# Kernel optimization log

Measured on AMD Instinct MI355X. Metric: run time of the kernel, lower is better.

## Reference

```python
import jax, jax.numpy as jnp
import numpy as np

B, C_IN, C_OUT, N, K = 8, 64, 128, 2048, 16
EPS = 1e-5  # torch BatchNorm2d default


def setup_inputs() -> dict:
    key = jax.random.key(0)
    ks = jax.random.split(key, 2)
    x = jax.random.normal(ks[0], (B, C_IN, N, 1), dtype=jnp.float32)
    # Conv2d(2*C_IN, C_OUT, 1) kaiming_normal weight, zero bias; 1x1 kernel -> [C_OUT, 2*C_IN]
    W = jax.random.normal(ks[1], (C_OUT, 2 * C_IN), dtype=jnp.float32) * np.float32(np.sqrt(2.0 / (2 * C_IN)))
    b = jnp.zeros((C_OUT,), jnp.float32)
    gamma = jnp.ones((C_OUT,), jnp.float32)   # BN weight filled with 1
    beta = jnp.zeros((C_OUT,), jnp.float32)   # BN bias zeroed
    return {"x": x, "W": W, "b": b, "gamma": gamma, "beta": beta, "k": K}


def reference(x, W, b, gamma, beta, k):
    # x: [B, C, N, 1]
    xs = x[..., 0]                              # [B, C, N]
    feats = jnp.transpose(xs, (0, 2, 1))        # [B, N, C]
    # knn: pairwise_distance = -||xi||^2 + 2 xi.xj - ||xj||^2 (negative sq dist)
    sq = jnp.sum(xs * xs, axis=1)               # [B, N]
    gram = jnp.einsum('bcn,bcm->bnm', xs, xs)   # [B, N, N]
    pd = 2.0 * gram - sq[:, :, None] - sq[:, None, :]
    idx = jax.lax.top_k(pd, k)[1]               # [B, N, k] neighbor indices
    # gather: x_j = neighbor features, x_i = center features broadcast over k
    x_j = jnp.take_along_axis(feats[:, None, :, :], idx[:, :, :, None], axis=2)  # [B, N, k, C]
    x_i = feats[:, :, None, :]                  # [B, N, 1, C]
    e = jnp.concatenate([jnp.broadcast_to(x_i, x_j.shape), x_j - x_i], axis=-1)  # [B, N, k, 2C]
    # 1x1 conv (matmul over channels) + ReLU
    h = jax.nn.relu(jnp.einsum('bnkc,oc->bnko', e, W) + b)  # [B, N, k, O]
    # BatchNorm2d in training mode: batch stats over (B, N, k), biased variance
    mean = jnp.mean(h, axis=(0, 1, 2))
    var = jnp.mean(jnp.square(h - mean), axis=(0, 1, 2))
    h = (h - mean) * jax.lax.rsqrt(var + EPS) * gamma + beta
    # max over neighbors, back to [B, O, N, 1]
    out = jnp.max(h, axis=2)                    # [B, N, O]
    return jnp.transpose(out, (0, 2, 1))[..., None]
```

## Files before the change

kernel.cpp:

```cpp
#include <hip/hip_runtime.h>
#include <math.h>

#define BB 8
#define CIN 64
#define CO 128
#define NPT 2048
#define KK 16
#define EPSV 1e-5f
#define LOSCALE 2048.0f

typedef unsigned int u32;
typedef unsigned long long u64;
typedef _Float16 f16x8 __attribute__((ext_vector_type(8)));
typedef float f32x4 __attribute__((ext_vector_type(4)));

__global__ __launch_bounds__(256) void k_prep_pv(
    const float* __restrict__ x, const float* __restrict__ W,
    const float* __restrict__ bias, float* __restrict__ sq,
    _Float16* __restrict__ xh, _Float16* __restrict__ xl,
    float* __restrict__ p, float* __restrict__ v) {
  __shared__ float tile[64][65];
  __shared__ float tileT[64][68];
  __shared__ float psum[4][64];
  int bid = blockIdx.x;
  int b = bid >> 5;
  int n0 = (bid & 31) << 6;
  int tid = threadIdx.x;
  int q = tid >> 6, lo = tid & 63;
#pragma unroll
  for (int i = 0; i < 16; ++i) {
    int c = i * 4 + q;
    tile[c][lo] = x[((size_t)(b * CIN + c)) * NPT + n0 + lo];
  }
  __syncthreads();
  float ps = 0.f;
#pragma unroll
  for (int i = 0; i < 16; ++i) {
    float t = tile[q * 16 + i][lo];
    ps += t * t;
  }
  psum[q][lo] = ps;
#pragma unroll
  for (int i = 0; i < 16; ++i) {
    int ni = i * 4 + q;
    float val = tile[lo][ni];
    tileT[ni][lo] = val;
    size_t o = ((size_t)(b * NPT + n0 + ni)) * CIN + lo;
    _Float16 h = (_Float16)val;
    xh[o] = h;
    xl[o] = (_Float16)((val - (float)h) * LOSCALE);
  }
  __syncthreads();
  if (q == 0) {
    sq[(size_t)b * NPT + n0 + lo] = psum[0][lo] + psum[1][lo] + psum[2][lo] + psum[3][lo];
  }
  int o = tid & 127, hh = tid >> 7;
  const float4* W1 = (const float4*)&W[o * 2 * CIN];
  const float4* W2 = (const float4*)&W[o * 2 * CIN + CIN];
  float bo = bias[o];
#pragma unroll 2
  for (int t = 0; t < 32; ++t) {
    int node = t * 2 + hh;
    float a1 = 0.f, a2 = 0.f;
#pragma unroll
    for (int c4 = 0; c4 < 16; ++c4) {
      float4 xv = *(const float4*)&tileT[node][c4 * 4];
      float4 w1 = W1[c4];
      float4 w2 = W2[c4];
      a1 += xv.x * w1.x + xv.y * w1.y + xv.z * w1.z + xv.w * w1.w;
      a2 += xv.x * w2.x + xv.y * w2.y + xv.z * w2.z + xv.w * w2.w;
    }
    size_t gn = ((size_t)(b * NPT + n0 + node)) * CO + o;
    p[gn] = a1 - a2 + bo;
    v[gn] = a2;
  }
}

__global__ __launch_bounds__(1024) void k_dist_topk(
    const _Float16* __restrict__ xh, const _Float16* __restrict__ xl,
    const float* __restrict__ sq, float* p_mx,
    const float* __restrict__ v, float* __restrict__ psums,
    float* __restrict__ psqs) {
  __shared__ uint4 tiles[16][2][256];
  __shared__ float submax[16][64];
  __shared__ float2 cand[16][96];
  __shared__ int cnt[16];
  __shared__ float tauf[16];

  int bid = (blockIdx.x & 7) * 128 + (blockIdx.x >> 3);
  int b = bid >> 7;
  int rt = (bid & 127) << 4;
  int tid = threadIdx.x;
  int w = tid >> 6, lane = tid & 63;
  int lr = lane & 15, lg = lane >> 4;
  const _Float16* xhb = xh + (size_t)b * NPT * CIN;
  const _Float16* xlb = xl + (size_t)b * NPT * CIN;
  const float* sqb = sq + (size_t)b * NPT;

  if (tid < 16) cnt[tid] = 0;

  const size_t arow = (size_t)(rt + lr) * CIN + lg * 8;
  f16x8 ah0 = *(const f16x8*)(xhb + arow);
  f16x8 ah1 = *(const f16x8*)(xhb + arow + 32);
  f16x8 al0 = *(const f16x8*)(xlb + arow);
  f16x8 al1 = *(const f16x8*)(xlb + arow + 32);
  float4 sqr = *(const float4*)(sqb + rt + lg * 4);
  float sqrv[4] = {sqr.x, sqr.y, sqr.z, sqr.w};
  float csqs[8];
#pragma unroll
  for (int t = 0; t < 8; ++t) csqs[t] = sqb[(w * 8 + t) * 16 + lr];

  const char* xhB = (const char*)xhb;
  const char* xlB = (const char*)xlb;
  const int su = (lane ^ ((lane >> 3) & 7)) * 16;

#define ISSUE_TILE(T)                                                          \
  {                                                                            \
    const int tb_ = (w * 8 + (T)) * 2048;                                      \
    uint4* buf_ = &tiles[w][(T) & 1][0];                                       \
    __builtin_amdgcn_global_load_lds((const uint4*)(xhB + tb_ + su),           \
                                     buf_, 16, 0, 0);                          \
    __builtin_amdgcn_global_load_lds((const uint4*)(xhB + tb_ + 1024 + su),    \
                                     buf_ + 64, 16, 0, 0);                     \
    __builtin_amdgcn_global_load_lds((const uint4*)(xlB + tb_ + su),           \
                                     buf_ + 128, 16, 0, 0);                    \
    __builtin_amdgcn_global_load_lds((const uint4*)(xlB + tb_ + 1024 + su),    \
                                     buf_ + 192, 16, 0, 0);                    \
  }

  ISSUE_TILE(0)
  ISSUE_TILE(1)

  const int uh0 = lr * 8 + (lg ^ (lr & 7));
  const int uh1 = lr * 8 + ((lg + 4) ^ (lr & 7));
  float vals[32];

#pragma unroll
  for (int t = 0; t < 8; ++t) {
    if (t < 7) { asm volatile("s_waitcnt vmcnt(4)" ::: "memory"); }
    else       { asm volatile("s_waitcnt vmcnt(0)" ::: "memory"); }
    __builtin_amdgcn_sched_barrier(0);
    const uint4* bufr = &tiles[w][t & 1][0];
    f16x8 bh0 = *(const f16x8*)(bufr + uh0);
    f16x8 bh1 = *(const f16x8*)(bufr + uh1);
    f16x8 bl0 = *(const f16x8*)(bufr + 128 + uh0);
    f16x8 bl1 = *(const f16x8*)(bufr + 128 + uh1);
    asm volatile("s_waitcnt lgkmcnt(0)" ::: "memory");
    __builtin_amdgcn_sched_barrier(0);
    if (t == 0) ISSUE_TILE(2)
    if (t == 1) ISSUE_TILE(3)
    if (t == 2) ISSUE_TILE(4)
    if (t == 3) ISSUE_TILE(5)
    if (t == 4) ISSUE_TILE(6)
    if (t == 5) ISSUE_TILE(7)
    f32x4 acc0 = {0.f, 0.f, 0.f, 0.f};
    f32x4 acc1 = {0.f, 0.f, 0.f, 0.f};
    acc1 = __builtin_amdgcn_mfma_f32_16x16x32_f16(ah0, bl0, acc1, 0, 0, 0);
    acc1 = __builtin_amdgcn_mfma_f32_16x16x32_f16(al0, bh0, acc1, 0, 0, 0);
    acc1 = __builtin_amdgcn_mfma_f32_16x16x32_f16(ah1, bl1, acc1, 0, 0, 0);
    acc1 = __builtin_amdgcn_mfma_f32_16x16x32_f16(al1, bh1, acc1, 0, 0, 0);
    acc0 = __builtin_amdgcn_mfma_f32_16x16x32_f16(ah0, bh0, acc0, 0, 0, 0);
    acc0 = __builtin_amdgcn_mfma_f32_16x16x32_f16(ah1, bh1, acc0, 0, 0, 0);
    const float k2 = 2.0f / LOSCALE;
#pragma unroll
    for (int q = 0; q < 4; ++q) {
      vals[t * 4 + q] = fmaf(acc1[q], k2, 2.f * acc0[q]) - (sqrv[q] + csqs[t]);
    }
  }
#undef ISSUE_TILE

  float rmax[4];
#pragma unroll
  for (int q = 0; q < 4; ++q) {
    float m = vals[q];
#pragma unroll
    for (int t = 1; t < 8; ++t) m = fmaxf(m, vals[t * 4 + q]);
    m = fmaxf(m, __shfl_xor(m, 1, 64));
    m = fmaxf(m, __shfl_xor(m, 2, 64));
    rmax[q] = m;
  }
  if ((lr & 3) == 0) {
    int pool = w * 4 + (lr >> 2);
#pragma unroll
    for (int q = 0; q < 4; ++q) submax[lg * 4 + q][pool] = rmax[q];
  }
  __syncthreads();

  {
    u32 ou = __float_as_uint(submax[w][lane]);
    ou = (ou & 0x80000000u) ? ~ou : (ou | 0x80000000u);
    u32 lo = 0u;
#pragma unroll
    for (int s2 = 31; s2 >= 16; --s2) {
      u32 cd = lo | (1u << s2);
      u64 bal = __ballot(ou >= cd);
      if (__popcll(bal) >= KK) lo = cd;
    }
    u32 tb = (lo & 0x80000000u) ? (lo ^ 0x80000000u) : ~lo;
    if (lane == 0) tauf[w] = __uint_as_float(tb);
  }
  __syncthreads();

  {
    float tq[4];
#pragma unroll
    for (int q = 0; q < 4; ++q) tq[q] = tauf[lg * 4 + q];
#pragma unroll
    for (int t = 0; t < 8; ++t) {
#pragma unroll
      for (int q = 0; q < 4; ++q) {
        float vv = vals[t * 4 + q];
        if (vv >= tq[q]) {
          int r = lg * 4 + q;
          int pos = atomicAdd(&cnt[r], 1);
          if (pos < 96) cand[r][pos] = make_float2(vv, __int_as_float((w * 8 + t) * 16 + lr));
        }
      }
    }
  }
  __syncthreads();

  int total = cnt[w];
  if (total > 96) total = 96;
  const float NINF = -__builtin_inff();
  float cv = NINF;
  int ci = 0x7FFFFFFF;
  int n1 = total < 64 ? total : 64;
  if (lane < n1) {
    float2 pr = cand[w][lane];
    cv = pr.x; ci = __float_as_int(pr.y);
  }

#define PSORT(KMAX)                                                        \
  _Pragma("unroll") for (int k = 2; k <= (KMAX); k <<= 1) {                \
    _Pragma("unroll") for (int j = k >> 1; j > 0; j >>= 1) {               \
      float pv = __shfl_xor(cv, j, 64);                                    \
      int pi = __shfl_xor(ci, j, 64);                                      \
      bool up = (lane & k) != 0;                                           \
      bool lw = (lane & j) == 0;                                           \
      bool gt = (cv > pv) || (cv == pv && ci < pi);                        \
      bool keep = (lw != up) ? gt : !gt;                                   \
      cv = keep ? cv : pv;                                                 \
      ci = keep ? ci : pi;                                                 \
    }                                                                      \
  }

  if (total > 32) {
    PSORT(64)
    if (total > 64) {
      if (lane >= 16) {
        int src2 = 48 + lane;
        if (src2 < total) {
          float2 pr = cand[w][src2];
          cv = pr.x; ci = __float_as_int(pr.y);
        } else { cv = NINF; ci = 0x7FFFFFFF; }
      }
      PSORT(64)
    }
  } else {
    PSORT(32)
  }
#undef PSORT

  {
    int jj[16];
#pragma unroll
    for (int k = 0; k < KK; ++k) jj[k] = __shfl(ci, k, 64) & (NPT - 1);
    size_t gn = (size_t)(b * NPT + rt + w);
    const float* vb = v + (size_t)b * NPT * CO;
    float2 p2 = *(const float2*)(p_mx + gn * CO + lane * 2);
    float2 s2 = {0.f, 0.f}, q2 = {0.f, 0.f}, m2 = {-1e30f, -1e30f};
#pragma unroll
    for (int k = 0; k < KK; ++k) {
      float2 v2 = *(const float2*)(vb + (size_t)jj[k] * CO + lane * 2);
      float h0 = fmaxf(p2.x + v2.x, 0.f);
      float h1 = fmaxf(p2.y + v2.y, 0.f);
      s2.x += h0; s2.y += h1;
      q2.x += h0 * h0; q2.y += h1 * h1;
      m2.x = fmaxf(m2.x, h0); m2.y = fmaxf(m2.y, h1);
    }
    *(float2*)(p_mx + gn * CO + lane * 2) = m2;
    float* sp = (float*)tiles;
    *(float2*)(sp + w * 128 + lane * 2) = s2;
    *(float2*)(sp + 2048 + w * 128 + lane * 2) = q2;
  }
  __syncthreads();
  if (tid < CO) {
    float* sp = (float*)tiles;
    float ts = 0.f, tq = 0.f;
#pragma unroll
    for (int i = 0; i < 16; ++i) { ts += sp[i * 128 + tid]; tq += sp[2048 + i * 128 + tid]; }
    int obid = b * 128 + (rt >> 4);
    psums[(size_t)obid * CO + tid] = ts;
    psqs[(size_t)obid * CO + tid] = tq;
  }
}

__global__ __launch_bounds__(64) void k_final(
    const float* __restrict__ psums, const float* __restrict__ psqs,
    const float* __restrict__ gamma, const float* __restrict__ beta,
    float* __restrict__ scale, float* __restrict__ shift) {
  int o = blockIdx.x;
  int t = threadIdx.x;
  float s = 0.f, q = 0.f;
  for (int i = t; i < BB * (NPT / 16); i += 64) {
    s += psums[(size_t)i * CO + o];
    q += psqs[(size_t)i * CO + o];
  }
#pragma unroll
  for (int d = 32; d >= 1; d >>= 1) {
    s += __shfl_down(s, d, 64);
    q += __shfl_down(q, d, 64);
  }
  if (t == 0) {
    const float M = (float)(BB * NPT * KK);
    float mean = s / M;
    float var = q / M - mean * mean;
    float sc = gamma[o] * rsqrtf(var + EPSV);
    scale[o] = sc;
    shift[o] = beta[o] - mean * sc;
  }
}

__global__ __launch_bounds__(256) void k_out_fast(
    const float* __restrict__ mxb, const float* __restrict__ scale,
    const float* __restrict__ shift, float* __restrict__ out) {
  __shared__ float ob[32][132];
  int bid = blockIdx.x;
  int b = bid >> 6;
  int n0 = (bid & 63) << 5;
  int tid = threadIdx.x;
  int o4 = tid & 31, ns = tid >> 5;
  float4 sc = *(const float4*)(scale + o4 * 4);
  float4 sh = *(const float4*)(shift + o4 * 4);
#pragma unroll
  for (int g = 0; g < 4; ++g) {
    int node = g * 8 + ns;
    size_t po = (size_t)(b * NPT + n0 + node) * CO + o4 * 4;
    float4 mx = *(const float4*)(mxb + po);
    float4 r;
    r.x = mx.x * sc.x + sh.x;
    r.y = mx.y * sc.y + sh.y;
    r.z = mx.z * sc.z + sh.z;
    r.w = mx.w * sc.w + sh.w;
    *(float4*)&ob[node][o4 * 4] = r;
  }
  __syncthreads();
  int ni = tid & 31, oh = tid >> 5;
#pragma unroll
  for (int pass = 0; pass < 16; ++pass) {
    int o = pass * 8 + oh;
    out[((size_t)(b * CO + o)) * NPT + n0 + ni] = ob[ni][o];
  }
}

extern "C" void kernel_launch(void* const* d_in, const int* in_sizes, int n_in,
                              void* d_out, int out_size, void* d_ws, size_t ws_size,
                              hipStream_t stream) {
  const float* x = (const float*)d_in[0];
  const float* W = (const float*)d_in[1];
  const float* bias = (const float*)d_in[2];
  const float* gamma = (const float*)d_in[3];
  const float* beta = (const float*)d_in[4];
  float* out = (float*)d_out;

  char* ws = (char*)d_ws;
  size_t off = 0;
  auto alloc = [&](size_t bytes) {
    void* ptr = ws + off;
    off += (bytes + 255) & ~(size_t)255;
    return ptr;
  };
  _Float16* xh = (_Float16*)alloc(sizeof(_Float16) * BB * NPT * CIN);
  _Float16* xl = (_Float16*)alloc(sizeof(_Float16) * BB * NPT * CIN);
  float* sq = (float*)alloc(sizeof(float) * BB * NPT);
  float* p = (float*)alloc(sizeof(float) * BB * NPT * CO);
  float* v = (float*)alloc(sizeof(float) * BB * NPT * CO);
  float* psums = (float*)alloc(sizeof(float) * BB * (NPT / 16) * CO);
  float* psqs = (float*)alloc(sizeof(float) * BB * (NPT / 16) * CO);
  float* scale = (float*)alloc(sizeof(float) * CO);
  float* shift = (float*)alloc(sizeof(float) * CO);
  (void)ws_size; (void)in_sizes; (void)n_in; (void)out_size;

  hipLaunchKernelGGL(k_prep_pv, dim3(BB * (NPT / 64)), dim3(256), 0, stream,
                     x, W, bias, sq, xh, xl, p, v);
  hipLaunchKernelGGL(k_dist_topk, dim3(BB * (NPT / 16)), dim3(1024), 0, stream,
                     xh, xl, sq, p, v, psums, psqs);
  hipLaunchKernelGGL(k_final, dim3(CO), dim3(64), 0, stream, psums, psqs, gamma, beta, scale, shift);
  hipLaunchKernelGGL(k_out_fast, dim3(BB * (NPT / 32)), dim3(256), 0, stream, p, scale, shift, out);
}
```

Baseline: 107.4 us.

## Compute per-point conv projections with split-fp16 MFMA instead of scalar FMA

The per-point linear projections p = (W1-W2)x + b and v = W2 x move from a scalar fp32 dot-product loop to MFMA 16x16x32 f16 instructions. Both operands are split into hi/lo fp16 parts to approximate fp32 accuracy, and the lo*lo term is dropped. A new small kernel pre-splits the weights (W1-W2 and W2) into hi/lo fp16 once per call. This cuts the scalar FLOP cost in k_prep_pv and removes the transposed fp32 LDS tile. The cost is an extra kernel launch and slightly reduced precision from the dropped cross term.

```diff
diff --git a/kernel.cpp b/kernel.cpp
--- a/kernel.cpp
+++ b/kernel.cpp
@@ -14,14 +14,33 @@
 typedef _Float16 f16x8 __attribute__((ext_vector_type(8)));
 typedef float f32x4 __attribute__((ext_vector_type(4)));
 
+__global__ __launch_bounds__(256) void k_wsplit(
+    const float* __restrict__ W, _Float16* __restrict__ wdh,
+    _Float16* __restrict__ wdl, _Float16* __restrict__ w2h,
+    _Float16* __restrict__ w2l) {
+  int i = blockIdx.x * 256 + threadIdx.x;
+  int o = i >> 6, c = i & 63;
+  float w1 = W[o * 2 * CIN + c];
+  float w2 = W[o * 2 * CIN + CIN + c];
+  float wd = w1 - w2;
+  _Float16 h2 = (_Float16)w2;
+  w2h[i] = h2;
+  w2l[i] = (_Float16)((w2 - (float)h2) * LOSCALE);
+  _Float16 hd = (_Float16)wd;
+  wdh[i] = hd;
+  wdl[i] = (_Float16)((wd - (float)hd) * LOSCALE);
+}
+
 __global__ __launch_bounds__(256) void k_prep_pv(
-    const float* __restrict__ x, const float* __restrict__ W,
-    const float* __restrict__ bias, float* __restrict__ sq,
-    _Float16* __restrict__ xh, _Float16* __restrict__ xl,
-    float* __restrict__ p, float* __restrict__ v) {
+    const float* __restrict__ x, const float* __restrict__ bias,
+    const _Float16* __restrict__ wdh, const _Float16* __restrict__ wdl,
+    const _Float16* __restrict__ w2h, const _Float16* __restrict__ w2l,
+    float* __restrict__ sq, _Float16* __restrict__ xh,
+    _Float16* __restrict__ xl, float* __restrict__ p, float* __restrict__ v) {
   __shared__ float tile[64][65];
-  __shared__ float tileT[64][68];
   __shared__ float psum[4][64];
+  __shared__ _Float16 xhp[64][72];
+  __shared__ _Float16 xlp[64][72];
   int bid = blockIdx.x;
   int b = bid >> 5;
   int n0 = (bid & 31) << 6;
@@ -44,35 +63,58 @@
   for (int i = 0; i < 16; ++i) {
     int ni = i * 4 + q;
     float val = tile[lo][ni];
-    tileT[ni][lo] = val;
     size_t o = ((size_t)(b * NPT + n0 + ni)) * CIN + lo;
     _Float16 h = (_Float16)val;
+    _Float16 l = (_Float16)((val - (float)h) * LOSCALE);
     xh[o] = h;
-    xl[o] = (_Float16)((val - (float)h) * LOSCALE);
-  }
-  __syncthreads();
+    xl[o] = l;
+    xhp[ni][lo] = h;
+    xlp[ni][lo] = l;
+  }
   if (q == 0) {
     sq[(size_t)b * NPT + n0 + lo] = psum[0][lo] + psum[1][lo] + psum[2][lo] + psum[3][lo];
   }
-  int o = tid & 127, hh = tid >> 7;
-  const float4* W1 = (const float4*)&W[o * 2 * CIN];
-  const float4* W2 = (const float4*)&W[o * 2 * CIN + CIN];
-  float bo = bias[o];
-#pragma unroll 2
-  for (int t = 0; t < 32; ++t) {
-    int node = t * 2 + hh;
-    float a1 = 0.f, a2 = 0.f;
-#pragma unroll
-    for (int c4 = 0; c4 < 16; ++c4) {
-      float4 xv = *(const float4*)&tileT[node][c4 * 4];
-      float4 w1 = W1[c4];
-      float4 w2 = W2[c4];
-      a1 += xv.x * w1.x + xv.y * w1.y + xv.z * w1.z + xv.w * w1.w;
-      a2 += xv.x * w2.x + xv.y * w2.y + xv.z * w2.z + xv.w * w2.w;
-    }
-    size_t gn = ((size_t)(b * NPT + n0 + node)) * CO + o;
-    p[gn] = a1 - a2 + bo;
-    v[gn] = a2;
+  __syncthreads();
+
+  int w = tid >> 6, lane = tid & 63;
+  int lr = lane & 15, lg = lane >> 4;
+  f16x8 ah0 = *(const f16x8*)&xhp[w * 16 + lr][lg * 8];
+  f16x8 ah1 = *(const f16x8*)&xhp[w * 16 + lr][lg * 8 + 32];
+  f16x8 al0 = *(const f16x8*)&xlp[w * 16 + lr][lg * 8];
+  f16x8 al1 = *(const f16x8*)&xlp[w * 16 + lr][lg * 8 + 32];
+  const float kinv = 1.0f / LOSCALE;
+#pragma unroll 1
+  for (int ot = 0; ot < 8; ++ot) {
+    int orow = ot * 16 + lr;
+    const f16x8 bdh0 = *(const f16x8*)(wdh + orow * 64 + lg * 8);
+    const f16x8 bdh1 = *(const f16x8*)(wdh + orow * 64 + lg * 8 + 32);
+    const f16x8 bdl0 = *(const f16x8*)(wdl + orow * 64 + lg * 8);
+    const f16x8 bdl1 = *(const f16x8*)(wdl + orow * 64 + lg * 8 + 32);
+    const f16x8 b2h0 = *(const f16x8*)(w2h + orow * 64 + lg * 8);
+    const f16x8 b2h1 = *(const f16x8*)(w2h + orow * 64 + lg * 8 + 32);
+    const f16x8 b2l0 = *(const f16x8*)(w2l + orow * 64 + lg * 8);
+    const f16x8 b2l1 = *(const f16x8*)(w2l + orow * 64 + lg * 8 + 32);
+    float bo = bias[orow];
+    f32x4 pa0 = {0.f, 0.f, 0.f, 0.f}, pa1 = {0.f, 0.f, 0.f, 0.f};
+    f32x4 va0 = {0.f, 0.f, 0.f, 0.f}, va1 = {0.f, 0.f, 0.f, 0.f};
+    pa1 = __builtin_amdgcn_mfma_f32_16x16x32_f16(ah0, bdl0, pa1, 0, 0, 0);
+    pa1 = __builtin_amdgcn_mfma_f32_16x16x32_f16(al0, bdh0, pa1, 0, 0, 0);
+    pa1 = __builtin_amdgcn_mfma_f32_16x16x32_f16(ah1, bdl1, pa1, 0, 0, 0);
+    pa1 = __builtin_amdgcn_mfma_f32_16x16x32_f16(al1, bdh1, pa1, 0, 0, 0);
+    pa0 = __builtin_amdgcn_mfma_f32_16x16x32_f16(ah0, bdh0, pa0, 0, 0, 0);
+    pa0 = __builtin_amdgcn_mfma_f32_16x16x32_f16(ah1, bdh1, pa0, 0, 0, 0);
+    va1 = __builtin_amdgcn_mfma_f32_16x16x32_f16(ah0, b2l0, va1, 0, 0, 0);
+    va1 = __builtin_amdgcn_mfma_f32_16x16x32_f16(al0, b2h0, va1, 0, 0, 0);
+    va1 = __builtin_amdgcn_mfma_f32_16x16x32_f16(ah1, b2l1, va1, 0, 0, 0);
+    va1 = __builtin_amdgcn_mfma_f32_16x16x32_f16(al1, b2h1, va1, 0, 0, 0);
+    va0 = __builtin_amdgcn_mfma_f32_16x16x32_f16(ah0, b2h0, va0, 0, 0, 0);
+    va0 = __builtin_amdgcn_mfma_f32_16x16x32_f16(ah1, b2h1, va0, 0, 0, 0);
+#pragma unroll
+    for (int qq = 0; qq < 4; ++qq) {
+      size_t gn = (size_t)(b * NPT + n0 + w * 16 + lg * 4 + qq) * CO + orow;
+      p[gn] = fmaf(pa1[qq], kinv, pa0[qq]) + bo;
+      v[gn] = fmaf(va1[qq], kinv, va0[qq]);
+    }
   }
 }
 
@@ -380,10 +422,15 @@
   float* psqs = (float*)alloc(sizeof(float) * BB * (NPT / 16) * CO);
   float* scale = (float*)alloc(sizeof(float) * CO);
   float* shift = (float*)alloc(sizeof(float) * CO);
+  _Float16* wdh = (_Float16*)alloc(sizeof(_Float16) * CO * CIN);
+  _Float16* wdl = (_Float16*)alloc(sizeof(_Float16) * CO * CIN);
+  _Float16* w2h = (_Float16*)alloc(sizeof(_Float16) * CO * CIN);
+  _Float16* w2l = (_Float16*)alloc(sizeof(_Float16) * CO * CIN);
   (void)ws_size; (void)in_sizes; (void)n_in; (void)out_size;
 
+  hipLaunchKernelGGL(k_wsplit, dim3(32), dim3(256), 0, stream, W, wdh, wdl, w2h, w2l);
   hipLaunchKernelGGL(k_prep_pv, dim3(BB * (NPT / 64)), dim3(256), 0, stream,
-                     x, W, bias, sq, xh, xl, p, v);
+                     x, bias, wdh, wdl, w2h, w2l, sq, xh, xl, p, v);
   hipLaunchKernelGGL(k_dist_topk, dim3(BB * (NPT / 16)), dim3(1024), 0, stream,
                      xh, xl, sq, p, v, psums, psqs);
   hipLaunchKernelGGL(k_final, dim3(CO), dim3(64), 0, stream, psums, psqs, gamma, beta, scale, shift);
```

Measured after the change: 100.8 us. 1.07x faster.
